# Performance work log

Measured on AMD Instinct MI355X. Metric: run time of the kernel, lower is better.

Reference implementation:

```python
import jax, jax.numpy as jnp
import numpy as np

N, IN_DIM, ERR_DIM, CAND, NR = 100000, 168, 24, 256, 4

def setup_inputs() -> dict:
    key = jax.random.key(0)
    k1, k2, k3, k4, k5 = jax.random.split(key, 5)
    return {
        "input": jax.random.normal(k1, (N, IN_DIM), dtype=jnp.float32),
        "error": jax.random.normal(k2, (N, ERR_DIM), dtype=jnp.float32),
        "weight_candidates": jax.random.normal(k3, (IN_DIM, CAND), dtype=jnp.float32),
        "bias_candidates": jax.random.normal(k4, (1, CAND), dtype=jnp.float32),
        "r": jax.random.uniform(k5, (NR,), dtype=jnp.float32),
    }

def reference(input, error, weight_candidates, bias_candidates, r):
    # candidates_state: [N, C] = sigmoid(X W + b)
    cand_state = jax.nn.sigmoid(input @ weight_candidates + bias_candidates)
    # E^T C: [D, C]; replaces per-(candidate,dim) tiny mm loop
    ec = jnp.einsum('nd,nc->dc', error, cand_state)
    # c^T c per candidate: [C]
    cc = jnp.sum(cand_state * cand_state, axis=0)
    # left_vector summed over dims: [C]
    left = jnp.sum(ec * ec, axis=0) / cc
    # sum over dims of e_dim^T e_dim: scalar
    ee = jnp.sum(error * error)
    # scores[idx, i] = sum_dim left - (1 - r_i) * right
    scores = left[:, None] - (1.0 - r)[None, :] * ee  # [C, NR]
    return scores
```

## Files before the change

### kernel.cpp

```cpp
#include <hip/hip_runtime.h>


#define N_ROWS 100000
#define IN_DIM 168
#define ERR_DIM 24
#define CAND 256

#define M_TILE 64
#define NT 1563
#define GRID_MAIN 512
#define XT_STRIDE 200
#define ST_STRIDE 72

typedef __bf16 bf16;
typedef bf16 bf16x4 __attribute__((ext_vector_type(4)));
typedef bf16 bf16x8 __attribute__((ext_vector_type(8)));
typedef float f32x4 __attribute__((ext_vector_type(4)));

#define EC_F 0
#define CC_F 8192
#define EE_F 8448
#define WP_BYTE 35840

__device__ __forceinline__ f32x4 mfma16(bf16x8 a, bf16x8 b, f32x4 c) {
    return __builtin_amdgcn_mfma_f32_16x16x32_bf16(a, b, c, 0, 0, 0);
}

__global__ __launch_bounds__(256) void prep_kernel(const float* __restrict__ W,
                                                   bf16* __restrict__ wp,
                                                   float* __restrict__ zero_region) {
    int tid = blockIdx.x * 256 + threadIdx.x;
    for (int i = tid; i < 8448; i += 6144) zero_region[i] = 0.0f;
    int ct  = tid / 384;
    int rem = tid % 384;
    int kt  = rem / 64;
    int l   = rem % 64;
    int c   = ct * 16 + (l & 15);
    int k0  = kt * 32 + (l >> 4) * 8;
    bf16x8 v;
#pragma unroll
    for (int j = 0; j < 8; ++j) {
        int k = k0 + j;
        float f = (k < IN_DIM) ? W[(size_t)k * CAND + c] : 0.0f;
        v[j] = (bf16)f;
    }
    *reinterpret_cast<bf16x8*>(wp + (size_t)tid * 8) = v;
}

__global__ __launch_bounds__(256) void fused_main(const float* __restrict__ X,
                                                  const float* __restrict__ E,
                                                  const float* __restrict__ B,
                                                  const bf16* __restrict__ wp,
                                                  float* __restrict__ ec_ws,
                                                  float* __restrict__ cc_ws,
                                                  float* __restrict__ ee_ws) {
    __shared__ bf16 XT[M_TILE * XT_STRIDE];
    __shared__ bf16 SigT[CAND * ST_STRIDE];
    __shared__ bf16 ET[32 * ST_STRIDE];
    __shared__ float red[8];

    const int tid  = threadIdx.x;
    const int wave = tid >> 6;
    const int lane = tid & 63;
    const int lo   = lane & 15;
    const int hi   = lane >> 4;
    const int wcol = wave * 64;

    bf16x8 wf[4][6];
#pragma unroll
    for (int cf = 0; cf < 4; ++cf)
#pragma unroll
        for (int kt = 0; kt < 6; ++kt) {
            int ct = (wcol >> 4) + cf;
            wf[cf][kt] = *reinterpret_cast<const bf16x8*>(wp + (((size_t)(ct * 6 + kt)) * 64 + lane) * 8);
        }

    float bv[4];
#pragma unroll
    for (int cf = 0; cf < 4; ++cf) bv[cf] = B[wcol + cf * 16 + lo];

    f32x4 ec_acc[2][4];
#pragma unroll
    for (int rf = 0; rf < 2; ++rf)
#pragma unroll
        for (int cf = 0; cf < 4; ++cf) ec_acc[rf][cf] = (f32x4){0.f, 0.f, 0.f, 0.f};
    float cc_acc[4] = {0.f, 0.f, 0.f, 0.f};
    float ee_acc = 0.f;

    for (int i = tid; i < 8 * ST_STRIDE; i += 256)
        ET[(24 + i / ST_STRIDE) * ST_STRIDE + (i % ST_STRIDE)] = (bf16)0.0f;

    for (int t = blockIdx.x; t < NT; t += GRID_MAIN) {
        const int row0 = t * M_TILE;
        __syncthreads();

        for (int i = tid; i < 64 * 42; i += 256) {
            int r = i / 42, c4 = i % 42;
            int gr = row0 + r;
            f32x4 v = {0.f, 0.f, 0.f, 0.f};
            if (gr < N_ROWS) v = *reinterpret_cast<const f32x4*>(X + (size_t)gr * IN_DIM + c4 * 4);
            bf16x4 pk = {(bf16)v.x, (bf16)v.y, (bf16)v.z, (bf16)v.w};
            *reinterpret_cast<bf16x4*>(&XT[r * XT_STRIDE + c4 * 4]) = pk;
        }
        for (int i = tid; i < 64 * 6; i += 256) {
            int r = i / 6, p = i % 6;
            bf16x4 z = {(bf16)0.f, (bf16)0.f, (bf16)0.f, (bf16)0.f};
            *reinterpret_cast<bf16x4*>(&XT[r * XT_STRIDE + IN_DIM + p * 4]) = z;
        }
        for (int i = tid; i < 64 * 6; i += 256) {
            int r = i / 6, p = i % 6;
            int gr = row0 + r;
            f32x4 v = {0.f, 0.f, 0.f, 0.f};
            if (gr < N_ROWS) v = *reinterpret_cast<const f32x4*>(E + (size_t)gr * ERR_DIM + p * 4);
            ee_acc += v.x * v.x + v.y * v.y + v.z * v.z + v.w * v.w;
            int d0 = p * 4;
            ET[(d0 + 0) * ST_STRIDE + r] = (bf16)v.x;
            ET[(d0 + 1) * ST_STRIDE + r] = (bf16)v.y;
            ET[(d0 + 2) * ST_STRIDE + r] = (bf16)v.z;
            ET[(d0 + 3) * ST_STRIDE + r] = (bf16)v.w;
        }
        __syncthreads();

        f32x4 acc[4][4];
#pragma unroll
        for (int mf = 0; mf < 4; ++mf)
#pragma unroll
            for (int cf = 0; cf < 4; ++cf) acc[mf][cf] = (f32x4){0.f, 0.f, 0.f, 0.f};
#pragma unroll
        for (int kt = 0; kt < 6; ++kt) {
            bf16x8 a[4];
#pragma unroll
            for (int mf = 0; mf < 4; ++mf)
                a[mf] = *reinterpret_cast<const bf16x8*>(&XT[(mf * 16 + lo) * XT_STRIDE + kt * 32 + hi * 8]);
#pragma unroll
            for (int mf = 0; mf < 4; ++mf)
#pragma unroll
                for (int cf = 0; cf < 4; ++cf)
                    acc[mf][cf] = mfma16(a[mf], wf[cf][kt], acc[mf][cf]);
        }

#pragma unroll
        for (int mf = 0; mf < 4; ++mf) {
            const int rb = row0 + mf * 16 + hi * 4;
#pragma unroll
            for (int cf = 0; cf < 4; ++cf) {
                f32x4 v = acc[mf][cf];
                float x0 = v.x + bv[cf], x1 = v.y + bv[cf], x2 = v.z + bv[cf], x3 = v.w + bv[cf];
                float s0 = 1.0f / (1.0f + __expf(-x0));
                float s1 = 1.0f / (1.0f + __expf(-x1));
                float s2 = 1.0f / (1.0f + __expf(-x2));
                float s3 = 1.0f / (1.0f + __expf(-x3));
                if (rb + 0 >= N_ROWS) s0 = 0.0f;
                if (rb + 1 >= N_ROWS) s1 = 0.0f;
                if (rb + 2 >= N_ROWS) s2 = 0.0f;
                if (rb + 3 >= N_ROWS) s3 = 0.0f;
                cc_acc[cf] += s0 * s0 + s1 * s1 + s2 * s2 + s3 * s3;
                bf16x4 pk = {(bf16)s0, (bf16)s1, (bf16)s2, (bf16)s3};
                *reinterpret_cast<bf16x4*>(&SigT[(wcol + cf * 16 + lo) * ST_STRIDE + mf * 16 + hi * 4]) = pk;
            }
        }

#pragma unroll
        for (int kt2 = 0; kt2 < 2; ++kt2) {
            bf16x8 ea[2], sb[4];
#pragma unroll
            for (int rf = 0; rf < 2; ++rf)
                ea[rf] = *reinterpret_cast<const bf16x8*>(&ET[(rf * 16 + lo) * ST_STRIDE + kt2 * 32 + hi * 8]);
#pragma unroll
            for (int cf = 0; cf < 4; ++cf)
                sb[cf] = *reinterpret_cast<const bf16x8*>(&SigT[(wcol + cf * 16 + lo) * ST_STRIDE + kt2 * 32 + hi * 8]);
#pragma unroll
            for (int rf = 0; rf < 2; ++rf)
#pragma unroll
                for (int cf = 0; cf < 4; ++cf)
                    ec_acc[rf][cf] = mfma16(ea[rf], sb[cf], ec_acc[rf][cf]);
        }
    }

#pragma unroll
    for (int rf = 0; rf < 2; ++rf)
#pragma unroll
        for (int cf = 0; cf < 4; ++cf)
#pragma unroll
            for (int r = 0; r < 4; ++r) {
                int d = rf * 16 + hi * 4 + r;
                if (d < ERR_DIM)
                    atomicAdd(&ec_ws[d * CAND + wcol + cf * 16 + lo], ec_acc[rf][cf][r]);
            }
#pragma unroll
    for (int cf = 0; cf < 4; ++cf) {
        float v = cc_acc[cf];
        v += __shfl_down(v, 32);
        v += __shfl_down(v, 16);
        if (lane < 16) atomicAdd(&cc_ws[wcol + cf * 16 + lane], v);
    }
#pragma unroll
    for (int off = 32; off > 0; off >>= 1) ee_acc += __shfl_down(ee_acc, off);
    if (lane == 0) red[wave] = ee_acc;
    __syncthreads();
    if (tid == 0) ee_ws[blockIdx.x] = red[0] + red[1] + red[2] + red[3];
}

__global__ __launch_bounds__(256) void finalize(const float* __restrict__ ec_ws,
                                                const float* __restrict__ cc_ws,
                                                const float* __restrict__ ee_ws,
                                                const float* __restrict__ r,
                                                float* __restrict__ out) {
    __shared__ float tmp[4];
    __shared__ float s_ee;
    int c = threadIdx.x;
    float p = ee_ws[c] + ee_ws[c + 256];
#pragma unroll
    for (int off = 32; off > 0; off >>= 1) p += __shfl_down(p, off);
    if ((c & 63) == 0) tmp[c >> 6] = p;
    __syncthreads();
    if (c == 0) s_ee = tmp[0] + tmp[1] + tmp[2] + tmp[3];
    __syncthreads();
    float ee = s_ee;
    float ccv = cc_ws[c];
    float left = 0.f;
#pragma unroll
    for (int d = 0; d < ERR_DIM; ++d) {
        float v = ec_ws[d * CAND + c];
        left += v * v;
    }
    left /= ccv;
#pragma unroll
    for (int i = 0; i < 4; ++i) out[c * 4 + i] = left - (1.0f - r[i]) * ee;
}

extern "C" void kernel_launch(void* const* d_in, const int* in_sizes, int n_in,
                              void* d_out, int out_size, void* d_ws, size_t ws_size,
                              hipStream_t stream) {
    const float* X = (const float*)d_in[0];
    const float* E = (const float*)d_in[1];
    const float* W = (const float*)d_in[2];
    const float* B = (const float*)d_in[3];
    const float* r = (const float*)d_in[4];

    float* wsf   = (float*)d_ws;
    float* ec_ws = wsf + EC_F;
    float* cc_ws = wsf + CC_F;
    float* ee_ws = wsf + EE_F;
    bf16*  wp    = (bf16*)((char*)d_ws + WP_BYTE);

    prep_kernel<<<24, 256, 0, stream>>>(W, wp, wsf);
    fused_main<<<GRID_MAIN, 256, 0, stream>>>(X, E, B, wp, ec_ws, cc_ws, ee_ws);
    finalize<<<1, 256, 0, stream>>>(ec_ws, cc_ws, ee_ws, r, (float*)d_out);
}
```

Before: 167.9 us.

## Batch global loads into registers, split atomic targets, fast sigmoid, occupancy hint

The X and E tile loads now go into registers before any conversion and LDS store, so more memory requests are in flight at once. The XT pad zeroing moves out of the tile loop. Sigmoid uses the hardware reciprocal approximation. launch_bounds asks for 2 blocks per CU. The ec and cc atomic accumulations are spread over 8 copies indexed by block to reduce contention, and finalize sums the copies. The costs are higher register pressure and a larger workspace to zero.

```diff
diff --git a/kernel.cpp b/kernel.cpp
--- a/kernel.cpp
+++ b/kernel.cpp
@@ -11,6 +11,7 @@
 #define GRID_MAIN 512
 #define XT_STRIDE 200
 #define ST_STRIDE 72
+#define NCOPY 8
 
 typedef __bf16 bf16;
 typedef bf16 bf16x4 __attribute__((ext_vector_type(4)));
@@ -18,19 +19,24 @@
 typedef float f32x4 __attribute__((ext_vector_type(4)));
 
 #define EC_F 0
-#define CC_F 8192
-#define EE_F 8448
-#define WP_BYTE 35840
+#define CC_F 49152
+#define EE_F 51200
+#define ZERO_N 51712
+#define WP_F 51712
 
 __device__ __forceinline__ f32x4 mfma16(bf16x8 a, bf16x8 b, f32x4 c) {
     return __builtin_amdgcn_mfma_f32_16x16x32_bf16(a, b, c, 0, 0, 0);
+}
+
+__device__ __forceinline__ float fast_sigmoid(float x) {
+    return __builtin_amdgcn_rcpf(1.0f + __expf(-x));
 }
 
 __global__ __launch_bounds__(256) void prep_kernel(const float* __restrict__ W,
                                                    bf16* __restrict__ wp,
                                                    float* __restrict__ zero_region) {
     int tid = blockIdx.x * 256 + threadIdx.x;
-    for (int i = tid; i < 8448; i += 6144) zero_region[i] = 0.0f;
+    for (int i = tid; i < ZERO_N; i += 6144) zero_region[i] = 0.0f;
     int ct  = tid / 384;
     int rem = tid % 384;
     int kt  = rem / 64;
@@ -47,13 +53,13 @@
     *reinterpret_cast<bf16x8*>(wp + (size_t)tid * 8) = v;
 }
 
-__global__ __launch_bounds__(256) void fused_main(const float* __restrict__ X,
-                                                  const float* __restrict__ E,
-                                                  const float* __restrict__ B,
-                                                  const bf16* __restrict__ wp,
-                                                  float* __restrict__ ec_ws,
-                                                  float* __restrict__ cc_ws,
-                                                  float* __restrict__ ee_ws) {
+__global__ __launch_bounds__(256, 2) void fused_main(const float* __restrict__ X,
+                                                     const float* __restrict__ E,
+                                                     const float* __restrict__ B,
+                                                     const bf16* __restrict__ wp,
+                                                     float* __restrict__ ec_ws,
+                                                     float* __restrict__ cc_ws,
+                                                     float* __restrict__ ee_ws) {
     __shared__ bf16 XT[M_TILE * XT_STRIDE];
     __shared__ bf16 SigT[CAND * ST_STRIDE];
     __shared__ bf16 ET[32 * ST_STRIDE];
@@ -89,35 +95,63 @@
 
     for (int i = tid; i < 8 * ST_STRIDE; i += 256)
         ET[(24 + i / ST_STRIDE) * ST_STRIDE + (i % ST_STRIDE)] = (bf16)0.0f;
+    {
+        bf16x4 z = {(bf16)0.f, (bf16)0.f, (bf16)0.f, (bf16)0.f};
+        for (int i = tid; i < 64 * 6; i += 256) {
+            int r = i / 6, p = i % 6;
+            *reinterpret_cast<bf16x4*>(&XT[r * XT_STRIDE + IN_DIM + p * 4]) = z;
+        }
+    }
 
     for (int t = blockIdx.x; t < NT; t += GRID_MAIN) {
         const int row0 = t * M_TILE;
         __syncthreads();
 
-        for (int i = tid; i < 64 * 42; i += 256) {
-            int r = i / 42, c4 = i % 42;
+        f32x4 xr[11], er[2];
+#pragma unroll
+        for (int j = 0; j < 11; ++j) {
+            int idx = tid + j * 256;
+            int r = idx / 42, c4 = idx - r * 42;
             int gr = row0 + r;
             f32x4 v = {0.f, 0.f, 0.f, 0.f};
-            if (gr < N_ROWS) v = *reinterpret_cast<const f32x4*>(X + (size_t)gr * IN_DIM + c4 * 4);
-            bf16x4 pk = {(bf16)v.x, (bf16)v.y, (bf16)v.z, (bf16)v.w};
-            *reinterpret_cast<bf16x4*>(&XT[r * XT_STRIDE + c4 * 4]) = pk;
-        }
-        for (int i = tid; i < 64 * 6; i += 256) {
-            int r = i / 6, p = i % 6;
-            bf16x4 z = {(bf16)0.f, (bf16)0.f, (bf16)0.f, (bf16)0.f};
-            *reinterpret_cast<bf16x4*>(&XT[r * XT_STRIDE + IN_DIM + p * 4]) = z;
-        }
-        for (int i = tid; i < 64 * 6; i += 256) {
-            int r = i / 6, p = i % 6;
+            if (idx < 2688 && gr < N_ROWS)
+                v = *reinterpret_cast<const f32x4*>(X + (size_t)gr * IN_DIM + c4 * 4);
+            xr[j] = v;
+        }
+#pragma unroll
+        for (int j = 0; j < 2; ++j) {
+            int idx = tid + j * 256;
+            int r = idx / 6, p = idx - r * 6;
             int gr = row0 + r;
             f32x4 v = {0.f, 0.f, 0.f, 0.f};
-            if (gr < N_ROWS) v = *reinterpret_cast<const f32x4*>(E + (size_t)gr * ERR_DIM + p * 4);
-            ee_acc += v.x * v.x + v.y * v.y + v.z * v.z + v.w * v.w;
-            int d0 = p * 4;
-            ET[(d0 + 0) * ST_STRIDE + r] = (bf16)v.x;
-            ET[(d0 + 1) * ST_STRIDE + r] = (bf16)v.y;
-            ET[(d0 + 2) * ST_STRIDE + r] = (bf16)v.z;
-            ET[(d0 + 3) * ST_STRIDE + r] = (bf16)v.w;
+            if (idx < 384 && gr < N_ROWS)
+                v = *reinterpret_cast<const f32x4*>(E + (size_t)gr * ERR_DIM + p * 4);
+            er[j] = v;
+        }
+
+#pragma unroll
+        for (int j = 0; j < 11; ++j) {
+            int idx = tid + j * 256;
+            if (idx < 2688) {
+                int r = idx / 42, c4 = idx - r * 42;
+                f32x4 v = xr[j];
+                bf16x4 pk = {(bf16)v.x, (bf16)v.y, (bf16)v.z, (bf16)v.w};
+                *reinterpret_cast<bf16x4*>(&XT[r * XT_STRIDE + c4 * 4]) = pk;
+            }
+        }
+#pragma unroll
+        for (int j = 0; j < 2; ++j) {
+            int idx = tid + j * 256;
+            if (idx < 384) {
+                int r = idx / 6, p = idx - r * 6;
+                f32x4 v = er[j];
+                ee_acc += v.x * v.x + v.y * v.y + v.z * v.z + v.w * v.w;
+                int d0 = p * 4;
+                ET[(d0 + 0) * ST_STRIDE + r] = (bf16)v.x;
+                ET[(d0 + 1) * ST_STRIDE + r] = (bf16)v.y;
+                ET[(d0 + 2) * ST_STRIDE + r] = (bf16)v.z;
+                ET[(d0 + 3) * ST_STRIDE + r] = (bf16)v.w;
+            }
         }
         __syncthreads();
 
@@ -145,11 +179,10 @@
 #pragma unroll
             for (int cf = 0; cf < 4; ++cf) {
                 f32x4 v = acc[mf][cf];
-                float x0 = v.x + bv[cf], x1 = v.y + bv[cf], x2 = v.z + bv[cf], x3 = v.w + bv[cf];
-                float s0 = 1.0f / (1.0f + __expf(-x0));
-                float s1 = 1.0f / (1.0f + __expf(-x1));
-                float s2 = 1.0f / (1.0f + __expf(-x2));
-                float s3 = 1.0f / (1.0f + __expf(-x3));
+                float s0 = fast_sigmoid(v.x + bv[cf]);
+                float s1 = fast_sigmoid(v.y + bv[cf]);
+                float s2 = fast_sigmoid(v.z + bv[cf]);
+                float s3 = fast_sigmoid(v.w + bv[cf]);
                 if (rb + 0 >= N_ROWS) s0 = 0.0f;
                 if (rb + 1 >= N_ROWS) s1 = 0.0f;
                 if (rb + 2 >= N_ROWS) s2 = 0.0f;
@@ -177,22 +210,24 @@
         }
     }
 
+    const int copy = blockIdx.x & (NCOPY - 1);
 #pragma unroll
     for (int rf = 0; rf < 2; ++rf)
 #pragma unroll
         for (int cf = 0; cf < 4; ++cf)
 #pragma unroll
-            for (int r = 0; r < 4; ++r) {
-                int d = rf * 16 + hi * 4 + r;
+            for (int rr = 0; rr < 4; ++rr) {
+                int d = rf * 16 + hi * 4 + rr;
                 if (d < ERR_DIM)
-                    atomicAdd(&ec_ws[d * CAND + wcol + cf * 16 + lo], ec_acc[rf][cf][r]);
+                    atomicAdd(&ec_ws[copy * (ERR_DIM * CAND) + d * CAND + wcol + cf * 16 + lo],
+                              ec_acc[rf][cf][rr]);
             }
 #pragma unroll
     for (int cf = 0; cf < 4; ++cf) {
         float v = cc_acc[cf];
         v += __shfl_down(v, 32);
         v += __shfl_down(v, 16);
-        if (lane < 16) atomicAdd(&cc_ws[wcol + cf * 16 + lane], v);
+        if (lane < 16) atomicAdd(&cc_ws[copy * CAND + wcol + cf * 16 + lane], v);
     }
 #pragma unroll
     for (int off = 32; off > 0; off >>= 1) ee_acc += __shfl_down(ee_acc, off);
@@ -217,11 +252,15 @@
     if (c == 0) s_ee = tmp[0] + tmp[1] + tmp[2] + tmp[3];
     __syncthreads();
     float ee = s_ee;
-    float ccv = cc_ws[c];
+    float ccv = 0.f;
+#pragma unroll
+    for (int cp = 0; cp < NCOPY; ++cp) ccv += cc_ws[cp * CAND + c];
     float left = 0.f;
 #pragma unroll
     for (int d = 0; d < ERR_DIM; ++d) {
-        float v = ec_ws[d * CAND + c];
+        float v = 0.f;
+#pragma unroll
+        for (int cp = 0; cp < NCOPY; ++cp) v += ec_ws[cp * (ERR_DIM * CAND) + d * CAND + c];
         left += v * v;
     }
     left /= ccv;
@@ -242,7 +281,7 @@
     float* ec_ws = wsf + EC_F;
     float* cc_ws = wsf + CC_F;
     float* ee_ws = wsf + EE_F;
-    bf16*  wp    = (bf16*)((char*)d_ws + WP_BYTE);
+    bf16*  wp    = (bf16*)(wsf + WP_F);
 
     prep_kernel<<<24, 256, 0, stream>>>(W, wp, wsf);
     fused_main<<<GRID_MAIN, 256, 0, stream>>>(X, E, B, wp, ec_ws, cc_ws, ee_ws);
```

Measured after the change: 166.4 us. No clear change (-0.9%).
